# Kernel tuning notes

Hardware: AMD Instinct MI355X
Metric: run time of the kernel (lower is better)

## Reference

```python
import jax, jax.numpy as jnp
import numpy as np

G, NPG = 100, 500
N = G * NPG            # 50000 nodes, contiguous equal-size graphs
IN, H = 128, 256
L = 3                  # num_layers
K = 3                  # knn k (loop=True -> self included)
E = 16 * N             # 800000 edges

def setup_inputs():
    key = jax.random.key(0)
    k = jax.random.split(key, 8)
    x = jax.random.normal(k[0], (N, IN), jnp.float32)
    batch = jnp.repeat(jnp.arange(G, dtype=jnp.int32), NPG)
    gid = jax.random.randint(k[1], (E,), 0, G)
    src = jax.random.randint(k[2], (E,), 0, NPG) + gid * NPG
    dst = jax.random.randint(k[3], (E,), 0, NPG) + gid * NPG
    edge_index = jnp.stack([src, dst]).astype(jnp.int32)
    def lin(kk, fin, fout):
        return (jax.random.normal(kk, (fin, fout), jnp.float32) / np.sqrt(fin)).astype(jnp.float32)
    inp = dict(x=x, edge_index=edge_index, batch=batch)
    inp["emb_W"] = lin(k[4], IN, H); inp["emb_b"] = jnp.zeros((H,), jnp.float32)
    inp["conv_W"] = jnp.stack([lin(jax.random.fold_in(k[5], i), H, H) for i in range(L)])
    inp["conv_b"] = jnp.zeros((L, H), jnp.float32)
    inp["fconv_W"] = jnp.stack([lin(jax.random.fold_in(k[6], i), H, H) for i in range(L)])
    inp["fconv_b"] = jnp.zeros((L, H), jnp.float32)
    inp["norm_w"] = jnp.ones((L, H), jnp.float32); inp["norm_b"] = jnp.zeros((L, H), jnp.float32); inp["norm_ms"] = jnp.ones((L, H), jnp.float32)
    inp["fnorm_w"] = jnp.ones((L, H), jnp.float32); inp["fnorm_b"] = jnp.zeros((L, H), jnp.float32); inp["fnorm_ms"] = jnp.ones((L, H), jnp.float32)
    inp["gate_W"] = lin(k[7], 2 * H, H); inp["gate_b"] = jnp.zeros((H,), jnp.float32)
    return inp

def _gcn_conv(h, src, dst, W, b):
    # GCNConv: add self loops, symmetric deg^-1/2 normalization
    m = h @ W                                     # [N,H]
    loop = jnp.arange(N, dtype=src.dtype)
    s2 = jnp.concatenate([src, loop]); d2 = jnp.concatenate([dst, loop])
    deg = jax.ops.segment_sum(jnp.ones_like(d2, jnp.float32), d2, num_segments=N)
    dinv = jnp.where(deg > 0, jax.lax.rsqrt(deg), 0.0)
    coef = (dinv[s2] * dinv[d2])[:, None]
    return jax.ops.segment_sum(m[s2] * coef, d2, num_segments=N) + b

def _graph_norm(x, batch, w, b, ms, cnt):
    # PyG GraphNorm: out = w * (x - ms*mean) / sqrt(var + eps) + b, per-graph stats
    mean = jax.ops.segment_sum(x, batch, num_segments=G) / cnt
    out = x - mean[batch] * ms
    var = jax.ops.segment_sum(out * out, batch, num_segments=G) / cnt
    return w * out * jax.lax.rsqrt(var + 1e-5)[batch] + b

def _knn_graph(x):
    # per-graph cosine knn, loop=True (self has sim 1 and is kept)
    xr = x.reshape(G, NPG, -1)
    xn = xr / (jnp.linalg.norm(xr, axis=-1, keepdims=True) + 1e-12)
    sim = jnp.einsum('gnh,gmh->gnm', xn, xn)      # [G,NPG,NPG]
    _, idx = jax.lax.top_k(sim, K)                # [G,NPG,K]
    offs = (jnp.arange(G) * NPG)[:, None, None]
    src = (idx + offs).reshape(-1)
    dst = jnp.broadcast_to(jnp.arange(N).reshape(G, NPG, 1), (G, NPG, K)).reshape(-1)
    return src.astype(jnp.int32), dst.astype(jnp.int32)

def reference(x, edge_index, batch, emb_W, emb_b, conv_W, conv_b, norm_w, norm_b, norm_ms, fconv_W, fconv_b, fnorm_w, fnorm_b, fnorm_ms, gate_W, gate_b):
    cnt = jax.ops.segment_sum(jnp.ones((N,), jnp.float32), batch, num_segments=G)[:, None]
    h = x @ emb_W + emb_b
    fsrc, fdst = _knn_graph(h)
    src, dst = edge_index[0], edge_index[1]
    all_x = []
    for i in range(L - 1):   # eval mode: dropout is identity
        prev = h
        h = _gcn_conv(h, src, dst, conv_W[i], conv_b[i])
        h = jax.nn.leaky_relu(_graph_norm(h, batch, norm_w[i], norm_b[i], norm_ms[i], cnt))
        f = _gcn_conv(h, fsrc, fdst, fconv_W[i], fconv_b[i])
        f = jax.nn.leaky_relu(_graph_norm(f, batch, fnorm_w[i], fnorm_b[i], fnorm_ms[i], cnt))
        gate = jax.nn.sigmoid(jnp.concatenate([h, f], axis=-1) @ gate_W + gate_b)
        h = gate * h + (1.0 - gate) * f + prev
        all_x.append(h)
    # faithful to source: for i in range(L): += pool(all_x[i-1])  (Python negative indexing!)
    gf = jnp.zeros((G, H), jnp.float32)
    for i in range(L):
        gf = gf + jax.ops.segment_sum(all_x[i - 1], batch, num_segments=G) / cnt
    return gf
```

## Files before the change

### kernel.cpp

```cpp
#include <hip/hip_runtime.h>
#include <math.h>

#define NN 50000
#define GG 100
#define NPGc 500
#define HH 256
#define IND 128

typedef __attribute__((ext_vector_type(8))) short short8v;
typedef __attribute__((ext_vector_type(4))) float f32x4;

__device__ __forceinline__ ushort f2bf(float f) {
    union { float f; unsigned u; } v; v.f = f;
    unsigned r = (v.u + 0x7fffu + ((v.u >> 16) & 1u)) >> 16;
    return (ushort)r;
}
__device__ __forceinline__ float bf2f(ushort h) {
    union { unsigned u; float f; } v; v.u = ((unsigned)h) << 16;
    return v.f;
}

__device__ __forceinline__ int swz(int row, int kidx) { return kidx ^ ((row & 7) << 3); }

__global__ void wcvt(const float* __restrict__ src, ushort* __restrict__ dst, int K, int N)
{
    int i = blockIdx.x * 256 + threadIdx.x;
    if (i < K * N) {
        int n = i / K, k = i % K;
        dst[i] = f2bf(src[(size_t)k * N + n]);
    }
}

__global__ __launch_bounds__(256)
void gemm_mfma(const float* __restrict__ A, const float* __restrict__ A2,
               const ushort* __restrict__ Wt, const float* __restrict__ bias,
               float* __restrict__ C, int M, int K, int lda, int mode,
               const float* __restrict__ hn, const float* __restrict__ fn,
               const float* __restrict__ prev)
{
    __shared__ ushort As[128][64];
    __shared__ ushort Bs[128][64];
    const int tid = threadIdx.x;
    const int lane = tid & 63;
    const int w = tid >> 6;
    const int wr = (w >> 1) * 64, wc = (w & 1) * 64;
    const int row0 = blockIdx.x * 128, col0 = blockIdx.y * 128;
    const int lr = lane & 15, lk = (lane >> 4) * 8;
    f32x4 acc[4][4] = {};

    for (int k0 = 0; k0 < K; k0 += 64) {
        __syncthreads();
        #pragma unroll
        for (int it = 0; it < 4; ++it) {
            int c = it * 256 + tid;
            int row = c >> 3, col = (c & 7) * 8;
            int gr = row0 + row; if (gr > M - 1) gr = M - 1;
            const float* Ap = A; int kk = k0 + col;
            if (A2 != nullptr && kk >= 256) { Ap = A2; kk -= 256; }
            const float* s = &Ap[(size_t)gr * lda + kk];
            float4 v0 = *(const float4*)s;
            float4 v1 = *(const float4*)(s + 4);
            union { ushort u[8]; int4 q; } pk;
            pk.u[0] = f2bf(v0.x); pk.u[1] = f2bf(v0.y); pk.u[2] = f2bf(v0.z); pk.u[3] = f2bf(v0.w);
            pk.u[4] = f2bf(v1.x); pk.u[5] = f2bf(v1.y); pk.u[6] = f2bf(v1.z); pk.u[7] = f2bf(v1.w);
            *(int4*)&As[row][swz(row, col)] = pk.q;
        }
        #pragma unroll
        for (int it = 0; it < 4; ++it) {
            int c = it * 256 + tid;
            int n = c >> 3, k = (c & 7) * 8;
            *(int4*)&Bs[n][swz(n, k)] = *(const int4*)&Wt[(size_t)(col0 + n) * K + k0 + k];
        }
        __syncthreads();
        #pragma unroll
        for (int ks = 0; ks < 2; ++ks) {
            short8v av[4], bv[4];
            #pragma unroll
            for (int m = 0; m < 4; ++m) {
                int rr = wr + m * 16 + lr;
                av[m] = *(const short8v*)&As[rr][swz(rr, ks * 32 + lk)];
            }
            #pragma unroll
            for (int n = 0; n < 4; ++n) {
                int rr = wc + n * 16 + lr;
                bv[n] = *(const short8v*)&Bs[rr][swz(rr, ks * 32 + lk)];
            }
            #pragma unroll
            for (int m = 0; m < 4; ++m)
                #pragma unroll
                for (int n = 0; n < 4; ++n)
                    acc[m][n] = __builtin_amdgcn_mfma_f32_16x16x32_bf16(av[m], bv[n], acc[m][n], 0, 0, 0);
        }
    }
    const int fr = (lane >> 4) * 4;
    if (mode == 0) {
        #pragma unroll
        for (int n = 0; n < 4; ++n) {
            int col = col0 + wc + n * 16 + lr;
            float bb = bias ? bias[col] : 0.f;
            #pragma unroll
            for (int m = 0; m < 4; ++m) {
                int rbase = row0 + wr + m * 16 + fr;
                #pragma unroll
                for (int r = 0; r < 4; ++r) {
                    int row = rbase + r;
                    if (row < M) C[(size_t)row * HH + col] = acc[m][n][r] + bb;
                }
            }
        }
    } else {
        #pragma unroll
        for (int n = 0; n < 4; ++n) {
            int col = col0 + wc + n * 16 + lr;
            float gb = bias[col];
            #pragma unroll
            for (int m = 0; m < 4; ++m) {
                int rbase = row0 + wr + m * 16 + fr;
                #pragma unroll
                for (int r = 0; r < 4; ++r) {
                    int row = rbase + r;
                    if (row < M) {
                        size_t o = (size_t)row * HH + col;
                        float z = acc[m][n][r] + gb;
                        float s = 1.f / (1.f + expf(-z));
                        C[o] = s * hn[o] + (1.f - s) * fn[o] + prev[o];
                    }
                }
            }
        }
    }
}

__global__ __launch_bounds__(256)
void row_norm_hl(const float* __restrict__ h, ushort* __restrict__ xh, ushort* __restrict__ xl)
{
    int n = blockIdx.x, c = threadIdx.x;
    float v = h[(size_t)n * HH + c];
    __shared__ float red[256];
    red[c] = v * v;
    __syncthreads();
    for (int s = 128; s > 0; s >>= 1) {
        if (c < s) red[c] += red[c + s];
        __syncthreads();
    }
    float norm = sqrtf(red[0]);
    float xn = v / (norm + 1e-12f);
    ushort hi = f2bf(xn);
    xh[(size_t)n * HH + c] = hi;
    xl[(size_t)n * HH + c] = f2bf(xn - bf2f(hi));
}

__device__ __forceinline__ bool tk_better(float va, int ia, float vb, int ib)
{
    return (va > vb) || (va == vb && ia < ib);
}

__device__ __forceinline__ void ins3(float v, int i,
                                     float& a0, int& b0, float& a1, int& b1,
                                     float& a2, int& b2)
{
    if (tk_better(v, i, a0, b0))      { a2 = a1; b2 = b1; a1 = a0; b1 = b0; a0 = v; b0 = i; }
    else if (tk_better(v, i, a1, b1)) { a2 = a1; b2 = b1; a1 = v;  b1 = i; }
    else if (tk_better(v, i, a2, b2)) { a2 = v;  b2 = i; }
}

__device__ __forceinline__ void merge3(float& v0, float& v1, float& v2,
                                       int& i0, int& i1, int& i2, int off)
{
    float w0 = __shfl_xor(v0, off), w1 = __shfl_xor(v1, off), w2 = __shfl_xor(v2, off);
    int   j0 = __shfl_xor(i0, off), j1 = __shfl_xor(i1, off), j2 = __shfl_xor(i2, off);
    float avv[3] = { v0, v1, v2 }, bvv[3] = { w0, w1, w2 };
    int   aii[3] = { i0, i1, i2 }, bii[3] = { j0, j1, j2 };
    float rv[3]; int ri[3];
    int p = 0, q = 0;
    #pragma unroll
    for (int t = 0; t < 3; ++t) {
        bool takeA = tk_better(avv[p], aii[p], bvv[q], bii[q]);
        rv[t] = takeA ? avv[p] : bvv[q];
        ri[t] = takeA ? aii[p] : bii[q];
        if (takeA) ++p; else ++q;
    }
    v0 = rv[0]; v1 = rv[1]; v2 = rv[2];
    i0 = ri[0]; i1 = ri[1]; i2 = ri[2];
}

__global__ __launch_bounds__(256, 2)
void simtopk(const ushort* __restrict__ xnh, const ushort* __restrict__ xnl,
             int* __restrict__ fsrc)
{
    __shared__ ushort Ash[128][64], Asl[128][64], Bsh[128][64], Bsl[128][64];
    const int bid = blockIdx.x;
    const int xcd = bid & 7;
    const int rb  = (bid >> 3) & 3;
    const int g   = (bid >> 5) * 8 + xcd;
    if (g >= GG) return;
    const int row0 = rb * 128;
    const int tid = threadIdx.x;
    const int lane = tid & 63;
    const int w = tid >> 6;
    const int wrow = w * 32;
    const int lr = lane & 15;
    const int hi4 = lane >> 4;
    const int lk = hi4 * 8;
    const size_t base = (size_t)g * NPGc * HH;

    float tv0[2][4], tv1[2][4], tv2[2][4];
    int   ti0[2][4], ti1[2][4], ti2[2][4];
    #pragma unroll
    for (int m = 0; m < 2; ++m)
        #pragma unroll
        for (int r = 0; r < 4; ++r) {
            tv0[m][r] = tv1[m][r] = tv2[m][r] = -2.f;
            ti0[m][r] = ti1[m][r] = ti2[m][r] = 0x7fffffff;
        }

    for (int ct = 0; ct < 4; ++ct) {
        const int col0 = ct * 128;
        f32x4 acc[2][8] = {};
        for (int k0 = 0; k0 < HH; k0 += 64) {
            __syncthreads();
            #pragma unroll
            for (int it = 0; it < 4; ++it) {
                int c = it * 256 + tid;
                int rr = c >> 3, kc = (c & 7) * 8;
                int grow = row0 + rr; if (grow > NPGc - 1) grow = NPGc - 1;
                const size_t o = base + (size_t)grow * HH + k0 + kc;
                *(int4*)&Ash[rr][swz(rr, kc)] = *(const int4*)(xnh + o);
                *(int4*)&Asl[rr][swz(rr, kc)] = *(const int4*)(xnl + o);
            }
            #pragma unroll
            for (int it = 0; it < 4; ++it) {
                int c = it * 256 + tid;
                int rr = c >> 3, kc = (c & 7) * 8;
                int gcol = col0 + rr; if (gcol > NPGc - 1) gcol = NPGc - 1;
                const size_t o = base + (size_t)gcol * HH + k0 + kc;
                *(int4*)&Bsh[rr][swz(rr, kc)] = *(const int4*)(xnh + o);
                *(int4*)&Bsl[rr][swz(rr, kc)] = *(const int4*)(xnl + o);
            }
            __syncthreads();
            #pragma unroll
            for (int ks = 0; ks < 2; ++ks) {
                short8v ah[2], al[2], bh[8], bl[8];
                #pragma unroll
                for (int m = 0; m < 2; ++m) {
                    int rr = wrow + m * 16 + lr;
                    ah[m] = *(const short8v*)&Ash[rr][swz(rr, ks * 32 + lk)];
                    al[m] = *(const short8v*)&Asl[rr][swz(rr, ks * 32 + lk)];
                }
                #pragma unroll
                for (int n = 0; n < 8; ++n) {
                    int rr = n * 16 + lr;
                    bh[n] = *(const short8v*)&Bsh[rr][swz(rr, ks * 32 + lk)];
                    bl[n] = *(const short8v*)&Bsl[rr][swz(rr, ks * 32 + lk)];
                }
                #pragma unroll
                for (int m = 0; m < 2; ++m)
                    #pragma unroll
                    for (int n = 0; n < 8; ++n) {
                        acc[m][n] = __builtin_amdgcn_mfma_f32_16x16x32_bf16(ah[m], bh[n], acc[m][n], 0, 0, 0);
                        acc[m][n] = __builtin_amdgcn_mfma_f32_16x16x32_bf16(ah[m], bl[n], acc[m][n], 0, 0, 0);
                        acc[m][n] = __builtin_amdgcn_mfma_f32_16x16x32_bf16(al[m], bh[n], acc[m][n], 0, 0, 0);
                    }
            }
        }
        #pragma unroll
        for (int m = 0; m < 2; ++m)
            #pragma unroll
            for (int n = 0; n < 8; ++n) {
                int col = col0 + n * 16 + lr;
                if (col < NPGc) {
                    #pragma unroll
                    for (int r = 0; r < 4; ++r)
                        ins3(acc[m][n][r], col,
                             tv0[m][r], ti0[m][r], tv1[m][r], ti1[m][r], tv2[m][r], ti2[m][r]);
                }
            }
    }

    #pragma unroll
    for (int m = 0; m < 2; ++m)
        #pragma unroll
        for (int r = 0; r < 4; ++r) {
            #pragma unroll
            for (int off = 1; off <= 8; off <<= 1)
                merge3(tv0[m][r], tv1[m][r], tv2[m][r],
                       ti0[m][r], ti1[m][r], ti2[m][r], off);
        }

    if (lr == 0) {
        #pragma unroll
        for (int m = 0; m < 2; ++m)
            #pragma unroll
            for (int r = 0; r < 4; ++r) {
                int row = row0 + wrow + m * 16 + hi4 * 4 + r;
                if (row < NPGc) {
                    int rg = g * NPGc + row;
                    fsrc[rg * 3 + 0] = g * NPGc + ti0[m][r];
                    fsrc[rg * 3 + 1] = g * NPGc + ti1[m][r];
                    fsrc[rg * 3 + 2] = g * NPGc + ti2[m][r];
                }
            }
    }
}

__global__ void hist_kernel(const int* __restrict__ dst, int* __restrict__ cnt, int nE)
{
    int e = blockIdx.x * 256 + threadIdx.x;
    if (e < nE) atomicAdd(&cnt[dst[e]], 1);
}

__global__ void scan1_kernel(const int* __restrict__ in, int* __restrict__ out,
                             int* __restrict__ bsum, int n)
{
    __shared__ int sh[256];
    int t = threadIdx.x;
    int i = blockIdx.x * 256 + t;
    int v = (i < n) ? in[i] : 0;
    sh[t] = v;
    __syncthreads();
    for (int s = 1; s < 256; s <<= 1) {
        int tv = (t >= s) ? sh[t - s] : 0;
        __syncthreads();
        sh[t] += tv;
        __syncthreads();
    }
    if (i < n) out[i] = sh[t] - v;
    if (t == 255) bsum[blockIdx.x] = sh[255];
}

__global__ void scan2_kernel(int* __restrict__ bsum, int nb)
{
    __shared__ int sh[256];
    int t = threadIdx.x;
    int v = (t < nb) ? bsum[t] : 0;
    sh[t] = v;
    __syncthreads();
    for (int s = 1; s < 256; s <<= 1) {
        int tv = (t >= s) ? sh[t - s] : 0;
        __syncthreads();
        sh[t] += tv;
        __syncthreads();
    }
    if (t < nb) bsum[t] = sh[t] - v;
}

__global__ void scan3_kernel(int* __restrict__ out, const int* __restrict__ bsum, int n)
{
    int i = blockIdx.x * 256 + threadIdx.x;
    if (i < n) out[i] += bsum[blockIdx.x];
}

__global__ void fill_kernel(const int* __restrict__ src, const int* __restrict__ dst,
                            const int* __restrict__ row_ptr, int* __restrict__ cursor,
                            int* __restrict__ sorted_src, int nE)
{
    int e = blockIdx.x * 256 + threadIdx.x;
    if (e < nE) {
        int d = dst[e];
        int pos = row_ptr[d] + atomicAdd(&cursor[d], 1);
        sorted_src[pos] = src[e];
    }
}

__global__ void dinv_kernel(const int* __restrict__ cnt, float* __restrict__ dinv, int n)
{
    int i = blockIdx.x * 256 + threadIdx.x;
    if (i < n) dinv[i] = rsqrtf((float)cnt[i] + 1.0f);
}

__global__ __launch_bounds__(256)
void gcn_gather(const float* __restrict__ m, const int* __restrict__ row_ptr,
                const int* __restrict__ cnt, const int* __restrict__ srcs,
                const float* __restrict__ dinv, const float* __restrict__ bias,
                float* __restrict__ out)
{
    int n = blockIdx.x, c = threadIdx.x;
    float dn = dinv[n];
    float acc = m[(size_t)n * HH + c] * dn;
    int s0 = row_ptr[n], e0 = s0 + cnt[n];
    for (int e = s0; e < e0; ++e) {
        int s = srcs[e];
        acc += m[(size_t)s * HH + c] * dinv[s];
    }
    out[(size_t)n * HH + c] = acc * dn + bias[c];
}

__global__ __launch_bounds__(256)
void fgcn_gather(const float* __restrict__ m, const int* __restrict__ fsrc,
                 const float* __restrict__ bias, float* __restrict__ out)
{
    int n = blockIdx.x, c = threadIdx.x;
    int s0 = fsrc[n * 3], s1 = fsrc[n * 3 + 1], s2 = fsrc[n * 3 + 2];
    float acc = m[(size_t)n * HH + c] + m[(size_t)s0 * HH + c]
              + m[(size_t)s1 * HH + c] + m[(size_t)s2 * HH + c];
    out[(size_t)n * HH + c] = 0.25f * acc + bias[c];
}

__global__ __launch_bounds__(256)
void norm_stats(const float* __restrict__ x, float* __restrict__ S1, float* __restrict__ S2)
{
    int g = blockIdx.x, chunk = blockIdx.y, c = threadIdx.x;
    int r0 = chunk * 63, r1 = min(r0 + 63, NPGc);
    float s1 = 0.f, s2 = 0.f;
    for (int r = r0; r < r1; ++r) {
        float v = x[((size_t)(g * NPGc + r)) * HH + c];
        s1 += v; s2 += v * v;
    }
    atomicAdd(&S1[g * HH + c], s1);
    atomicAdd(&S2[g * HH + c], s2);
}

__global__ __launch_bounds__(256)
void norm_apply(float* __restrict__ x, const float* __restrict__ S1, const float* __restrict__ S2,
                const float* __restrict__ w, const float* __restrict__ b,
                const float* __restrict__ ms)
{
    int n = blockIdx.x, c = threadIdx.x;
    int g = n / NPGc;
    size_t o = (size_t)n * HH + c;
    float v = x[o];
    float mean = S1[g * HH + c] / (float)NPGc;
    float mm = mean * ms[c];
    float var = S2[g * HH + c] / (float)NPGc - 2.f * mm * mean + mm * mm;
    float outv = w[c] * (v - mm) * rsqrtf(var + 1e-5f) + b[c];
    x[o] = outv > 0.f ? outv : 0.01f * outv;
}

__global__ __launch_bounds__(256)
void pool_kernel(const float* __restrict__ X0, const float* __restrict__ X1,
                 float* __restrict__ out)
{
    int g = blockIdx.x, c = threadIdx.x;
    float s0 = 0.f, s1 = 0.f;
    for (int r = 0; r < NPGc; ++r) {
        size_t o = ((size_t)(g * NPGc + r)) * HH + c;
        s0 += X0[o];
        s1 += X1[o];
    }
    out[g * HH + c] = (s0 + 2.f * s1) / (float)NPGc;
}

__global__ void sentinel_kernel(float* out, int n)
{
    int i = blockIdx.x * 256 + threadIdx.x;
    if (i < n) out[i] = 12345.0f;
}

extern "C" void kernel_launch(void* const* d_in, const int* in_sizes, int n_in,
                              void* d_out, int out_size, void* d_ws, size_t ws_size,
                              hipStream_t stream)
{
    const float* x       = (const float*)d_in[0];
    const int* edge_idx  = (const int*)d_in[1];
    const float* emb_W   = (const float*)d_in[3];
    const float* emb_b   = (const float*)d_in[4];
    const float* conv_W  = (const float*)d_in[5];
    const float* conv_b  = (const float*)d_in[6];
    const float* fconv_W = (const float*)d_in[7];
    const float* fconv_b = (const float*)d_in[8];
    const float* norm_w  = (const float*)d_in[9];
    const float* norm_b  = (const float*)d_in[10];
    const float* norm_ms = (const float*)d_in[11];
    const float* fnorm_w = (const float*)d_in[12];
    const float* fnorm_b = (const float*)d_in[13];
    const float* fnorm_ms= (const float*)d_in[14];
    const float* gate_W  = (const float*)d_in[15];
    const float* gate_b  = (const float*)d_in[16];

    const int E = in_sizes[1] / 2;
    const int* esrc = edge_idx;
    const int* edst = edge_idx + E;

    const size_t NHf = (size_t)NN * HH;
    char* p = (char*)d_ws;
    auto alloc = [&](size_t bytes) { char* r = p; p += (bytes + 255) & ~(size_t)255; return r; };
    float* B0 = (float*)alloc(NHf * 4);
    float* B1 = (float*)alloc(NHf * 4);
    float* B2 = (float*)alloc(NHf * 4);
    float* B3 = (float*)alloc(NHf * 4);
    ushort* xnh = (ushort*)B2;
    ushort* xnl = xnh + NHf;
    int* sorted_src = (int*)alloc((size_t)E * 4);
    int* row_ptr    = (int*)alloc((size_t)NN * 4);
    int* deg_cnt    = (int*)alloc((size_t)NN * 4);
    int* cursor     = (int*)alloc((size_t)NN * 4);
    float* dinv     = (float*)alloc((size_t)NN * 4);
    int* fsrc       = (int*)alloc((size_t)NN * 3 * 4);
    float* S1       = (float*)alloc((size_t)GG * HH * 4);
    float* S2       = (float*)alloc((size_t)GG * HH * 4);
    int* bsum       = (int*)alloc(1024);
    ushort* wts     = (ushort*)alloc((size_t)425984 * 2);
    size_t needed = (size_t)(p - (char*)d_ws);
    if (ws_size < needed) {
        sentinel_kernel<<<(out_size + 255) / 256, 256, 0, stream>>>((float*)d_out, out_size);
        return;
    }
    ushort* embWt   = wts;
    ushort* convWt0 = wts + 32768;
    ushort* convWt1 = wts + 32768 + 65536;
    ushort* fconvWt0 = wts + 163840;
    ushort* fconvWt1 = wts + 163840 + 65536;
    ushort* gateWt  = wts + 294912;

    const int nScanB = (NN + 255) / 256;

    hipMemsetAsync(deg_cnt, 0, (size_t)NN * 4, stream);
    hipMemsetAsync(cursor, 0, (size_t)NN * 4, stream);

    wcvt<<<(32768 + 255) / 256, 256, 0, stream>>>(emb_W, embWt, IND, HH);
    wcvt<<<(65536 + 255) / 256, 256, 0, stream>>>(conv_W, convWt0, HH, HH);
    wcvt<<<(65536 + 255) / 256, 256, 0, stream>>>(conv_W + 65536, convWt1, HH, HH);
    wcvt<<<(65536 + 255) / 256, 256, 0, stream>>>(fconv_W, fconvWt0, HH, HH);
    wcvt<<<(65536 + 255) / 256, 256, 0, stream>>>(fconv_W + 65536, fconvWt1, HH, HH);
    wcvt<<<(131072 + 255) / 256, 256, 0, stream>>>(gate_W, gateWt, 2 * HH, HH);

    dim3 ggrid((NN + 127) / 128, 2);
    gemm_mfma<<<ggrid, 256, 0, stream>>>(x, nullptr, embWt, emb_b, B0, NN, IND, IND, 0,
                                         nullptr, nullptr, nullptr);

    hist_kernel<<<(E + 255) / 256, 256, 0, stream>>>(edst, deg_cnt, E);
    scan1_kernel<<<nScanB, 256, 0, stream>>>(deg_cnt, row_ptr, bsum, NN);
    scan2_kernel<<<1, 256, 0, stream>>>(bsum, nScanB);
    scan3_kernel<<<nScanB, 256, 0, stream>>>(row_ptr, bsum, NN);
    fill_kernel<<<(E + 255) / 256, 256, 0, stream>>>(esrc, edst, row_ptr, cursor, sorted_src, E);
    dinv_kernel<<<(NN + 255) / 256, 256, 0, stream>>>(deg_cnt, dinv, NN);

    row_norm_hl<<<NN, 256, 0, stream>>>(B0, xnh, xnl);
    simtopk<<<416, 256, 0, stream>>>(xnh, xnl, fsrc);

    float* h  = B0;
    float* mb = B1;
    dim3 ngrid(GG, 8);
    for (int i = 0; i < 2; ++i) {
        const ushort* Wc = (i == 0) ? convWt0 : convWt1;
        const ushort* Wf = (i == 0) ? fconvWt0 : fconvWt1;
        const float* bc  = conv_b  + (size_t)i * HH;
        const float* bf  = fconv_b + (size_t)i * HH;
        gemm_mfma<<<ggrid, 256, 0, stream>>>(h, nullptr, Wc, nullptr, mb, NN, HH, HH, 0,
                                             nullptr, nullptr, nullptr);
        gcn_gather<<<NN, 256, 0, stream>>>(mb, row_ptr, deg_cnt, sorted_src, dinv, bc, B2);
        hipMemsetAsync(S1, 0, (size_t)2 * GG * HH * 4, stream);
        norm_stats<<<ngrid, 256, 0, stream>>>(B2, S1, S2);
        norm_apply<<<NN, 256, 0, stream>>>(B2, S1, S2, norm_w + i * HH, norm_b + i * HH,
                                           norm_ms + i * HH);
        gemm_mfma<<<ggrid, 256, 0, stream>>>(B2, nullptr, Wf, nullptr, mb, NN, HH, HH, 0,
                                             nullptr, nullptr, nullptr);
        fgcn_gather<<<NN, 256, 0, stream>>>(mb, fsrc, bf, B3);
        hipMemsetAsync(S1, 0, (size_t)2 * GG * HH * 4, stream);
        norm_stats<<<ngrid, 256, 0, stream>>>(B3, S1, S2);
        norm_apply<<<NN, 256, 0, stream>>>(B3, S1, S2, fnorm_w + i * HH, fnorm_b + i * HH,
                                           fnorm_ms + i * HH);
        gemm_mfma<<<ggrid, 256, 0, stream>>>(B2, B3, gateWt, gate_b, mb, NN, 2 * HH, HH, 1,
                                             B2, B3, h);
        float* t = h; h = mb; mb = t;
    }
    pool_kernel<<<GG, 256, 0, stream>>>(mb, h, (float*)d_out);
}
```

Measured before the change: 1.377 ms.

## Restructure kNN similarity top-k kernel with register-resident A rows and double-buffered B

The similarity/top-k kernel now gives each block 64 query rows instead of 128, doubling the grid to 832 blocks. Each wave holds its 16 A rows (hi and lo bf16 parts across all of K) in registers. Only the B tile is staged through a small double-buffered LDS array, with the next K-chunk loaded from global memory while the current chunk's MFMAs run. This cuts LDS footprint and per-iteration LDS traffic and adds parallelism. In exchange it uses more registers and re-reads B once per 64-row block instead of once per 128.

```diff
diff --git a/kernel.cpp b/kernel.cpp
--- a/kernel.cpp
+++ b/kernel.cpp
@@ -188,118 +188,123 @@
 void simtopk(const ushort* __restrict__ xnh, const ushort* __restrict__ xnl,
              int* __restrict__ fsrc)
 {
-    __shared__ ushort Ash[128][64], Asl[128][64], Bsh[128][64], Bsl[128][64];
+    __shared__ ushort Bs[2][2][128][36];
     const int bid = blockIdx.x;
     const int xcd = bid & 7;
-    const int rb  = (bid >> 3) & 3;
-    const int g   = (bid >> 5) * 8 + xcd;
+    const int rb  = (bid >> 3) & 7;
+    const int g   = (bid >> 6) * 8 + xcd;
     if (g >= GG) return;
-    const int row0 = rb * 128;
-    const int tid = threadIdx.x;
+    const int row0 = rb * 64;
+    const int tid  = threadIdx.x;
     const int lane = tid & 63;
-    const int w = tid >> 6;
-    const int wrow = w * 32;
-    const int lr = lane & 15;
-    const int hi4 = lane >> 4;
-    const int lk = hi4 * 8;
+    const int w    = tid >> 6;
+    const int lr   = lane & 15;
+    const int hi4  = lane >> 4;
     const size_t base = (size_t)g * NPGc * HH;
 
-    float tv0[2][4], tv1[2][4], tv2[2][4];
-    int   ti0[2][4], ti1[2][4], ti2[2][4];
+    int arow = row0 + w * 16 + lr; if (arow > NPGc - 1) arow = NPGc - 1;
+    const ushort* aph = xnh + base + (size_t)arow * HH + hi4 * 8;
+    const ushort* apl = xnl + base + (size_t)arow * HH + hi4 * 8;
+    short8v ah[8], al[8];
     #pragma unroll
-    for (int m = 0; m < 2; ++m)
-        #pragma unroll
-        for (int r = 0; r < 4; ++r) {
-            tv0[m][r] = tv1[m][r] = tv2[m][r] = -2.f;
-            ti0[m][r] = ti1[m][r] = ti2[m][r] = 0x7fffffff;
-        }
+    for (int kc = 0; kc < 8; ++kc) {
+        ah[kc] = *(const short8v*)(aph + kc * 32);
+        al[kc] = *(const short8v*)(apl + kc * 32);
+    }
+
+    const int scol = tid >> 1;
+    const int sq   = (tid & 1) * 2;
+
+    float tv0[4], tv1[4], tv2[4];
+    int   ti0[4], ti1[4], ti2[4];
+    #pragma unroll
+    for (int r = 0; r < 4; ++r) {
+        tv0[r] = tv1[r] = tv2[r] = -2.f;
+        ti0[r] = ti1[r] = ti2[r] = 0x7fffffff;
+    }
 
     for (int ct = 0; ct < 4; ++ct) {
         const int col0 = ct * 128;
-        f32x4 acc[2][8] = {};
-        for (int k0 = 0; k0 < HH; k0 += 64) {
+        int gcol = col0 + scol; if (gcol > NPGc - 1) gcol = NPGc - 1;
+        const ushort* sph = xnh + base + (size_t)gcol * HH + sq * 8;
+        const ushort* spl = xnl + base + (size_t)gcol * HH + sq * 8;
+
+        {
+            int4 h0 = *(const int4*)(sph);
+            int4 h1 = *(const int4*)(sph + 8);
+            int4 l0 = *(const int4*)(spl);
+            int4 l1 = *(const int4*)(spl + 8);
+            *(int4*)&Bs[0][0][scol][sq * 8]     = h0;
+            *(int4*)&Bs[0][0][scol][sq * 8 + 8] = h1;
+            *(int4*)&Bs[0][1][scol][sq * 8]     = l0;
+            *(int4*)&Bs[0][1][scol][sq * 8 + 8] = l1;
+        }
+        __syncthreads();
+
+        f32x4 acc[8] = {};
+        #pragma unroll
+        for (int kc = 0; kc < 8; ++kc) {
+            const int cur = kc & 1, nxt = cur ^ 1;
+            int4 h0, h1, l0, l1;
+            if (kc < 7) {
+                const ushort* nh = sph + (kc + 1) * 32;
+                const ushort* nl = spl + (kc + 1) * 32;
+                h0 = *(const int4*)(nh);
+                h1 = *(const int4*)(nh + 8);
+                l0 = *(const int4*)(nl);
+                l1 = *(const int4*)(nl + 8);
+            }
+            short8v bh[8], bl[8];
+            #pragma unroll
+            for (int n = 0; n < 8; ++n) {
+                int rr = n * 16 + lr;
+                bh[n] = *(const short8v*)&Bs[cur][0][rr][hi4 * 8];
+                bl[n] = *(const short8v*)&Bs[cur][1][rr][hi4 * 8];
+            }
+            #pragma unroll
+            for (int n = 0; n < 8; ++n) {
+                acc[n] = __builtin_amdgcn_mfma_f32_16x16x32_bf16(ah[kc], bh[n], acc[n], 0, 0, 0);
+                acc[n] = __builtin_amdgcn_mfma_f32_16x16x32_bf16(ah[kc], bl[n], acc[n], 0, 0, 0);
+                acc[n] = __builtin_amdgcn_mfma_f32_16x16x32_bf16(al[kc], bh[n], acc[n], 0, 0, 0);
+            }
+            if (kc < 7) {
+                *(int4*)&Bs[nxt][0][scol][sq * 8]     = h0;
+                *(int4*)&Bs[nxt][0][scol][sq * 8 + 8] = h1;
+                *(int4*)&Bs[nxt][1][scol][sq * 8]     = l0;
+                *(int4*)&Bs[nxt][1][scol][sq * 8 + 8] = l1;
+            }
             __syncthreads();
-            #pragma unroll
-            for (int it = 0; it < 4; ++it) {
-                int c = it * 256 + tid;
-                int rr = c >> 3, kc = (c & 7) * 8;
-                int grow = row0 + rr; if (grow > NPGc - 1) grow = NPGc - 1;
-                const size_t o = base + (size_t)grow * HH + k0 + kc;
-                *(int4*)&Ash[rr][swz(rr, kc)] = *(const int4*)(xnh + o);
-                *(int4*)&Asl[rr][swz(rr, kc)] = *(const int4*)(xnl + o);
-            }
-            #pragma unroll
-            for (int it = 0; it < 4; ++it) {
-                int c = it * 256 + tid;
-                int rr = c >> 3, kc = (c & 7) * 8;
-                int gcol = col0 + rr; if (gcol > NPGc - 1) gcol = NPGc - 1;
-                const size_t o = base + (size_t)gcol * HH + k0 + kc;
-                *(int4*)&Bsh[rr][swz(rr, kc)] = *(const int4*)(xnh + o);
-                *(int4*)&Bsl[rr][swz(rr, kc)] = *(const int4*)(xnl + o);
-            }
-            __syncthreads();
-            #pragma unroll
-            for (int ks = 0; ks < 2; ++ks) {
-                short8v ah[2], al[2], bh[8], bl[8];
+        }
+
+        #pragma unroll
+        for (int n = 0; n < 8; ++n) {
+            int col = col0 + n * 16 + lr;
+            if (col < NPGc) {
                 #pragma unroll
-                for (int m = 0; m < 2; ++m) {
-                    int rr = wrow + m * 16 + lr;
-                    ah[m] = *(const short8v*)&Ash[rr][swz(rr, ks * 32 + lk)];
-                    al[m] = *(const short8v*)&Asl[rr][swz(rr, ks * 32 + lk)];
-                }
-                #pragma unroll
-                for (int n = 0; n < 8; ++n) {
-                    int rr = n * 16 + lr;
-                    bh[n] = *(const short8v*)&Bsh[rr][swz(rr, ks * 32 + lk)];
-                    bl[n] = *(const short8v*)&Bsl[rr][swz(rr, ks * 32 + lk)];
-                }
-                #pragma unroll
-                for (int m = 0; m < 2; ++m)
-                    #pragma unroll
-                    for (int n = 0; n < 8; ++n) {
-                        acc[m][n] = __builtin_amdgcn_mfma_f32_16x16x32_bf16(ah[m], bh[n], acc[m][n], 0, 0, 0);
-                        acc[m][n] = __builtin_amdgcn_mfma_f32_16x16x32_bf16(ah[m], bl[n], acc[m][n], 0, 0, 0);
-                        acc[m][n] = __builtin_amdgcn_mfma_f32_16x16x32_bf16(al[m], bh[n], acc[m][n], 0, 0, 0);
-                    }
-            }
-        }
-        #pragma unroll
-        for (int m = 0; m < 2; ++m)
-            #pragma unroll
-            for (int n = 0; n < 8; ++n) {
-                int col = col0 + n * 16 + lr;
-                if (col < NPGc) {
-                    #pragma unroll
-                    for (int r = 0; r < 4; ++r)
-                        ins3(acc[m][n][r], col,
-                             tv0[m][r], ti0[m][r], tv1[m][r], ti1[m][r], tv2[m][r], ti2[m][r]);
-                }
-            }
+                for (int r = 0; r < 4; ++r)
+                    ins3(acc[n][r], col, tv0[r], ti0[r], tv1[r], ti1[r], tv2[r], ti2[r]);
+            }
+        }
     }
 
     #pragma unroll
-    for (int m = 0; m < 2; ++m)
+    for (int r = 0; r < 4; ++r) {
+        #pragma unroll
+        for (int off = 1; off <= 8; off <<= 1)
+            merge3(tv0[r], tv1[r], tv2[r], ti0[r], ti1[r], ti2[r], off);
+    }
+
+    if (lr == 0) {
         #pragma unroll
         for (int r = 0; r < 4; ++r) {
-            #pragma unroll
-            for (int off = 1; off <= 8; off <<= 1)
-                merge3(tv0[m][r], tv1[m][r], tv2[m][r],
-                       ti0[m][r], ti1[m][r], ti2[m][r], off);
-        }
-
-    if (lr == 0) {
-        #pragma unroll
-        for (int m = 0; m < 2; ++m)
-            #pragma unroll
-            for (int r = 0; r < 4; ++r) {
-                int row = row0 + wrow + m * 16 + hi4 * 4 + r;
-                if (row < NPGc) {
-                    int rg = g * NPGc + row;
-                    fsrc[rg * 3 + 0] = g * NPGc + ti0[m][r];
-                    fsrc[rg * 3 + 1] = g * NPGc + ti1[m][r];
-                    fsrc[rg * 3 + 2] = g * NPGc + ti2[m][r];
-                }
-            }
+            int row = row0 + w * 16 + hi4 * 4 + r;
+            if (row < NPGc) {
+                int rg = g * NPGc + row;
+                fsrc[rg * 3 + 0] = g * NPGc + ti0[r];
+                fsrc[rg * 3 + 1] = g * NPGc + ti1[r];
+                fsrc[rg * 3 + 2] = g * NPGc + ti2[r];
+            }
+        }
     }
 }
 
@@ -526,7 +531,7 @@
     dinv_kernel<<<(NN + 255) / 256, 256, 0, stream>>>(deg_cnt, dinv, NN);
 
     row_norm_hl<<<NN, 256, 0, stream>>>(B0, xnh, xnl);
-    simtopk<<<416, 256, 0, stream>>>(xnh, xnl, fsrc);
+    simtopk<<<832, 256, 0, stream>>>(xnh, xnl, fsrc);
 
     float* h  = B0;
     float* mb = B1;
```

After: 1.371 ms. Within noise of the previous version (-0.4%).
